# Performance work log

Hardware: AMD Instinct MI355X
Metric: run time of the kernel (lower is better)

## Reference

```python
import jax, jax.numpy as jnp
import numpy as np
from jax import lax

NUM_SIMS = 2048
NUM_BITS = 256   # == num_nodes
MID_DIM = 512
LN_EPS = 1e-5


def _net(x, w1, b1, gamma, beta, w2, b2):
    # BnMLP: Linear -> GELU (exact erf) -> LayerNorm -> Linear -> Sigmoid
    h = x @ w1 + b1                                   # [S, MID]
    h = jax.nn.gelu(h, approximate=False)
    mu = jnp.mean(h, axis=-1, keepdims=True)
    var = jnp.mean(jnp.square(h - mu), axis=-1, keepdims=True)
    h = (h - mu) * lax.rsqrt(var + LN_EPS) * gamma + beta
    return jax.nn.sigmoid(h @ w2 + b2)                # [S, NUM_BITS]


def setup_inputs() -> dict:
    key = jax.random.key(0)
    k_x, k_p, k_w1, k_w2 = jax.random.split(key, 4)
    xs_flt = jax.random.uniform(k_x, (NUM_SIMS, NUM_BITS), dtype=jnp.float32)
    # one random permutation of the nodes per simulation (th.randperm per sim)
    ids_ary = jax.vmap(lambda k: jax.random.permutation(k, NUM_BITS))(
        jax.random.split(k_p, NUM_SIMS)).astype(jnp.int32)   # [S, N]
    w1 = jax.random.normal(k_w1, (NUM_BITS, MID_DIM), jnp.float32) / np.sqrt(NUM_BITS)
    b1 = jnp.full((MID_DIM,), 1e-6, jnp.float32)
    gamma = jnp.ones((MID_DIM,), jnp.float32)
    beta = jnp.zeros((MID_DIM,), jnp.float32)
    w2 = jax.random.normal(k_w2, (MID_DIM, NUM_BITS), jnp.float32) * (0.1 / np.sqrt(MID_DIM))
    b2 = jnp.full((NUM_BITS,), 1e-6, jnp.float32)
    return {"xs_flt": xs_flt, "ids_ary": ids_ary, "w1": w1, "b1": b1,
            "gamma": gamma, "beta": beta, "w2": w2, "b2": b2}


def reference(xs_flt, ids_ary, w1, b1, gamma, beta, w2, b2):
    # gathers prob at (sim, ids[sim]) and writes ps broadcast over all rows at
    # columns ids (faithful to torch's `probs[:, ids] = ps` broadcast semantics).
    def step(probs, ids):
        out = _net(probs, w1, b1, gamma, beta, w2, b2)        # [S, N]
        ps = jnp.take_along_axis(out, ids[:, None], axis=1)[:, 0]  # [S]
        probs = probs.at[:, ids].set(ps)                      # broadcast over rows
        return probs, None

    probs, _ = lax.scan(step, xs_flt, ids_ary.T)              # scan over N nodes
    return probs
```

## Files before the change

kernel.cpp:

```cpp
#include <hip/hip_runtime.h>
#include <math.h>

#define S_ 2048
#define N_ 256
#define MID_ 512
#define NB_ 8
#define JSL_ 64
#define LN_EPS_ 1e-5f
#define NBLK_ 64
#define NSTEP_ 253
#define BSTRIDE_ 288
#define SLOT_F_ (NB_*BSTRIDE_)
#define TAGST_ 16
#define TAG_TARGET_ 0x0101010101010101ULL

typedef float f32x4 __attribute__((ext_vector_type(4)));
typedef float f32x2 __attribute__((ext_vector_type(2)));

__device__ __forceinline__ float gelu_exact(float x){
    return 0.5f * x * (1.0f + erff(x * 0.70710678118654752440f));
}


__global__ __launch_bounds__(256) void k_setup(
    const int* __restrict__ ids, const float* __restrict__ gamma,
    const float* __restrict__ beta, const float* __restrict__ w2,
    const float* __restrict__ b2,
    unsigned int* __restrict__ wmaskb, int* __restrict__ winners,
    float* __restrict__ A, float* __restrict__ Bc,
    int* __restrict__ tagw32, int* __restrict__ cnt, int* __restrict__ winner)
{
    __shared__ float ra[256], rb[256];
    __shared__ unsigned int mb[8];
    __shared__ int lk[N_];
    int bi = blockIdx.x, tid = threadIdx.x;

    if (tid < 32){
        int ii = bi*32 + tid;
        if (ii < NSTEP_*TAGST_*2) tagw32[ii] = 0;
    }
    if (bi == 0 && tid < 8) cnt[tid] = 0;
    if (bi == 0 && tid == 0) *winner = -1;

    if (tid < 8) mb[tid] = 0u;
    lk[tid] = -1;
    __syncthreads();
    #pragma unroll
    for (int m = 0; m < 8; m++){
        int k = tid + m*256;
        int c = ids[k*N_ + bi];
        atomicOr(&mb[c>>5], 1u << (c&31));
        if (bi < 3) atomicMax(&lk[c], k);
    }
    float a = 0.f, b = 0.f;
    for (int j = tid; j < MID_; j += 256){
        float v = w2[j*N_ + bi];
        a += gamma[j]*v;
        b += beta[j]*v;
    }
    ra[tid] = a; rb[tid] = b;
    __syncthreads();
    for (int off = 128; off > 0; off >>= 1){
        if (tid < off){ ra[tid] += ra[tid+off]; rb[tid] += rb[tid+off]; }
        __syncthreads();
    }
    if (tid == 0){ A[bi] = ra[0]; Bc[bi] = rb[0] + b2[bi]; }
    if (tid < 8) wmaskb[bi*8 + tid] = mb[tid];
    if (bi < 3) winners[bi*N_ + tid] = lk[tid];
}


__global__ __launch_bounds__(256) void k_fullW(
    const float* __restrict__ xs, const float* __restrict__ w1,
    const float* __restrict__ b1, const float* __restrict__ gamma,
    const float* __restrict__ beta, const float* __restrict__ w2,
    const float* __restrict__ b2, const int* __restrict__ winners,
    float* __restrict__ nv, int t)
{
    __shared__ float prow[4][N_];
    int tid = threadIdx.x;
    int r = tid >> 6, l = tid & 63;
    int c = blockIdx.x*4 + r;
    int kr = winners[t*N_ + c];
    int krow = kr < 0 ? 0 : kr;
    #pragma unroll
    for (int q = 0; q < 4; q++){
        int cc = l*4 + q;
        float v = xs[krow*N_ + cc];
        if (t > 0 && winners[cc] >= 0)      v = nv[cc];
        if (t > 1 && winners[N_ + cc] >= 0) v = nv[N_ + cc];
        prow[r][cc] = v;
    }
    float h[8];
    #pragma unroll
    for (int m = 0; m < 8; m++) h[m] = b1[l + 64*m];
    for (int cc = 0; cc < N_; cc++){
        float p = prow[r][cc];
        const float* w1r = w1 + cc*MID_;
        #pragma unroll
        for (int m = 0; m < 8; m++) h[m] = fmaf(p, w1r[l + 64*m], h[m]);
    }
    float s1 = 0.f, s2 = 0.f;
    #pragma unroll
    for (int m = 0; m < 8; m++){
        float g = gelu_exact(h[m]);
        h[m] = g; s1 += g; s2 += g*g;
    }
    #pragma unroll
    for (int off = 32; off > 0; off >>= 1){
        s1 += __shfl_xor(s1, off, 64);
        s2 += __shfl_xor(s2, off, 64);
    }
    float mu  = s1 * (1.f/MID_);
    float var = s2 * (1.f/MID_) - mu*mu;
    float inv = rsqrtf(var + LN_EPS_);
    float acc = 0.f;
    #pragma unroll
    for (int m = 0; m < 8; m++){
        int j = l + 64*m;
        float hn = (h[m] - mu)*inv*gamma[j] + beta[j];
        acc = fmaf(hn, w2[j*N_ + c], acc);
    }
    #pragma unroll
    for (int off = 32; off > 0; off >>= 1) acc += __shfl_xor(acc, off, 64);
    if (l == 0) nv[t*N_ + c] = 1.f/(1.f + expf(-(acc + b2[c])));
}


__global__ __launch_bounds__(512) void k_fast(
    const float* __restrict__ w1, const float* __restrict__ b1,
    const float* __restrict__ gamma, const float* __restrict__ w2,
    const float* __restrict__ A, const float* __restrict__ Bc,
    const unsigned int* __restrict__ wmaskb, const float* __restrict__ xs,
    const int* __restrict__ winners3, const float* __restrict__ nv,
    float* __restrict__ slots, unsigned long long* __restrict__ tagw,
    int* __restrict__ cnt, int* __restrict__ winner,
    float* __restrict__ out, int t0)
{
    __shared__ int s_role;
    __shared__ __attribute__((aligned(16))) float commonS[N_];
    __shared__ __attribute__((aligned(16))) float gvals[JSL_];
    __shared__ __attribute__((aligned(16))) float crow[N_];
    __shared__ float ws8[16];
    __shared__ float pst[NB_][2];
    __shared__ unsigned int wbits[(N_*N_)/32];

    int tid = threadIdx.x;

    if (tid == 0){
        int xcd;
        asm volatile("s_getreg_b32 %0, hwreg(HW_REG_XCC_ID)" : "=s"(xcd));
        xcd &= 7;
        int pos = atomicAdd(&cnt[xcd], 1);
        int role = -1;
        if (pos == NB_ - 1){
            int old = atomicCAS(winner, -1, xcd);
            if (old == -1) role = NB_ - 1;
        } else if (pos < NB_ - 1){
            int w;
            while ((w = atomicCAS(winner, -2, -2)) == -1)
                __builtin_amdgcn_s_sleep(2);
            if (w == xcd) role = pos;
        }
        s_role = role;
    }
    __syncthreads();
    int role = s_role;
    if (role < 0) return;
    int j0 = role * JSL_;

    int l = tid & 63, w = tid >> 6;
    int cg = l & 7;
    int jA = (w<<3) + (l>>3);
    int cB = w*32 + (l & 31);
    int khalf = l >> 5;

    float w1r[32];
    #pragma unroll
    for (int cc = 0; cc < 32; cc++)
        w1r[cc] = w1[(cg*32 + cc)*MID_ + j0 + jA];
    float g2r[32];
    #pragma unroll
    for (int kk = 0; kk < 32; kk++)
        g2r[kk] = gamma[j0 + khalf*32 + kk] * w2[(j0 + khalf*32 + kk)*N_ + cB];
    float b1v = b1[j0 + jA];

    for (int i = tid; i < (N_*N_)/32; i += 512) wbits[i] = wmaskb[i];
    if (tid < N_){
        float v = xs[tid];
        if (winners3[tid] >= 0)        v = nv[tid];
        if (winners3[N_ + tid] >= 0)   v = nv[N_ + tid];
        if (winners3[2*N_ + tid] >= 0) v = nv[2*N_ + tid];
        commonS[tid ^ (((tid>>5)&7)<<2)] = v;
    }
    float Ac  = (tid < N_) ? A[tid]  : 0.f;
    float Bcc = (tid < N_) ? Bc[tid] : 0.f;
    __syncthreads();

    for (int t = t0; t < N_; t++){
        int si = t - t0;
        float* slot = slots + si*SLOT_F_;
        float* myp  = slot + role*BSTRIDE_;
        {
            float a0=0.f, a1=0.f, a2=0.f, a3=0.f;
            #pragma unroll
            for (int cc = 0; cc < 8; cc++){
                f32x4 cv = *(const f32x4*)(&commonS[(cg*32 + cc*4) ^ (cg<<2)]);
                a0 = fmaf(w1r[cc*4+0], cv.x, a0);
                a1 = fmaf(w1r[cc*4+1], cv.y, a1);
                a2 = fmaf(w1r[cc*4+2], cv.z, a2);
                a3 = fmaf(w1r[cc*4+3], cv.w, a3);
            }
            float hp = (a0+a1) + (a2+a3);
            hp += __shfl_xor(hp, 1);
            hp += __shfl_xor(hp, 2);
            hp += __shfl_xor(hp, 4);
            float g = gelu_exact(hp + b1v);
            float s1 = g, s2 = g*g;
            s1 += __shfl_xor(s1, 8);  s2 += __shfl_xor(s2, 8);
            s1 += __shfl_xor(s1, 16); s2 += __shfl_xor(s2, 16);
            s1 += __shfl_xor(s1, 32); s2 += __shfl_xor(s2, 32);
            if (l == 0){ ws8[w*2] = s1; ws8[w*2+1] = s2; }
            if (cg == 0) gvals[jA] = g;
        }
        __syncthreads();
        {
            float p0=0.f, p1=0.f, p2=0.f, p3=0.f;
            #pragma unroll
            for (int kk = 0; kk < 8; kk++){
                f32x4 gv = *(const f32x4*)(&gvals[khalf*32 + kk*4]);
                p0 = fmaf(g2r[kk*4+0], gv.x, p0);
                p1 = fmaf(g2r[kk*4+1], gv.y, p1);
                p2 = fmaf(g2r[kk*4+2], gv.z, p2);
                p3 = fmaf(g2r[kk*4+3], gv.w, p3);
            }
            float p = (p0+p1) + (p2+p3);
            p += __shfl_xor(p, 32);
            if (l < 32) myp[cB] = p;
        }
        if (tid == 0){
            float S1 = 0.f, S2 = 0.f;
            #pragma unroll
            for (int ww = 0; ww < 8; ww++){ S1 += ws8[ww*2]; S2 += ws8[ww*2+1]; }
            f32x2 st; st.x = S1; st.y = S2;
            *(f32x2*)(myp + 256) = st;
        }
        asm volatile("s_waitcnt vmcnt(0)" ::: "memory");
        __syncthreads();
        {
            unsigned long long* tp = tagw + si*TAGST_;
            if (tid == 0) atomicAdd(tp, 1ULL << (8*role));
            if (tid < NB_){
                while (atomicAdd(tp, 0ULL) != TAG_TARGET_) {}
                f32x2 st = *(const f32x2*)(slot + tid*BSTRIDE_ + 256);
                pst[tid][0] = st.x; pst[tid][1] = st.y;
            }
        }
        __syncthreads();
        if (tid < N_){
            const float* sp = slot + tid;
            float s1 = 0.f;
            #pragma unroll
            for (int bb = 0; bb < NB_; bb++) s1 += sp[bb*BSTRIDE_];
            float S1 = 0.f, S2 = 0.f;
            #pragma unroll
            for (int bb = 0; bb < NB_; bb++){ S1 += pst[bb][0]; S2 += pst[bb][1]; }
            float mu  = S1 * (1.f/MID_);
            float var = S2 * (1.f/MID_) - mu*mu;
            float inv = rsqrtf(var + LN_EPS_);
            float s = inv*(s1 - mu*Ac) + Bcc;
            float o = 1.f/(1.f + expf(-s));
            if ((wbits[(t<<3) + (tid>>5)] >> (tid&31)) & 1u)
                commonS[tid ^ (((tid>>5)&7)<<2)] = o;
        }
        __syncthreads();
    }
    if (tid < N_) crow[tid] = commonS[tid ^ (((tid>>5)&7)<<2)];
    __syncthreads();
    {
        float* obase = out + (role*256)*N_;
        for (int i = tid; i < 256*(N_/4); i += 512){
            int rr = i >> 6, v4 = i & 63;
            *(f32x4*)(&obase[rr*N_ + v4*4]) = *(const f32x4*)(&crow[v4*4]);
        }
    }
}


extern "C" void kernel_launch(void* const* d_in, const int* in_sizes, int n_in,
                              void* d_out, int out_size, void* d_ws, size_t ws_size,
                              hipStream_t stream)
{
    const float* xs    = (const float*)d_in[0];
    const int*   ids   = (const int*)  d_in[1];
    const float* w1    = (const float*)d_in[2];
    const float* b1    = (const float*)d_in[3];
    const float* gamma = (const float*)d_in[4];
    const float* beta  = (const float*)d_in[5];
    const float* w2    = (const float*)d_in[6];
    const float* b2    = (const float*)d_in[7];
    float* out = (float*)d_out;

    float* ws      = (float*)d_ws;
    float* slots   = ws;
    float* nv      = ws + 582912;
    float* A       = ws + 583680;
    float* Bc      = ws + 583936;
    int*   winners = (int*)(ws + 584192);
    unsigned int* wmaskb = (unsigned int*)(ws + 584960);
    int*   tagw32  = (int*)(ws + 587008);
    unsigned long long* tagw = (unsigned long long*)tagw32;
    int*   cnt     = tagw32 + NSTEP_*TAGST_*2;
    int*   winner  = cnt + 8;

    k_setup<<<256, 256, 0, stream>>>(ids, gamma, beta, w2, b2, wmaskb, winners,
                                     A, Bc, tagw32, cnt, winner);

    for (int t = 0; t < 3; t++)
        k_fullW<<<64, 256, 0, stream>>>(xs, w1, b1, gamma, beta, w2, b2,
                                        winners, nv, t);

    k_fast<<<NBLK_, 512, 0, stream>>>(w1, b1, gamma, w2, A, Bc, wmaskb, xs,
                                      winners, nv, slots, tagw, cnt, winner,
                                      out, 3);
}
```

Measured before the change: 637.6 us.

## Reduce per-step partials with float atomics into one shared row

Each of the 8 cooperating blocks used to write its partial second-layer sums and LayerNorm statistics to a private slot. Readers then waited on a byte-packed tag and summed all 8 slots. Now every block atomically adds into a single accumulator row per step, signals an int counter, and each consuming wave spins on the counter itself, which removes one block-wide barrier. This cuts the per-step gather latency and barrier count on the sequential critical path, at the cost of contended float atomics and a non-deterministic summation order.

```diff
diff --git a/kernel.cpp b/kernel.cpp
--- a/kernel.cpp
+++ b/kernel.cpp
@@ -9,10 +9,8 @@
 #define LN_EPS_ 1e-5f
 #define NBLK_ 64
 #define NSTEP_ 253
-#define BSTRIDE_ 288
-#define SLOT_F_ (NB_*BSTRIDE_)
-#define TAGST_ 16
-#define TAG_TARGET_ 0x0101010101010101ULL
+#define AROW_ 288
+#define TAGW_ 32
 
 typedef float f32x4 __attribute__((ext_vector_type(4)));
 typedef float f32x2 __attribute__((ext_vector_type(2)));
@@ -28,17 +26,16 @@
     const float* __restrict__ b2,
     unsigned int* __restrict__ wmaskb, int* __restrict__ winners,
     float* __restrict__ A, float* __restrict__ Bc,
-    int* __restrict__ tagw32, int* __restrict__ cnt, int* __restrict__ winner)
+    float* __restrict__ accum, int* __restrict__ tagw32,
+    int* __restrict__ cnt, int* __restrict__ winner)
 {
     __shared__ float ra[256], rb[256];
     __shared__ unsigned int mb[8];
     __shared__ int lk[N_];
     int bi = blockIdx.x, tid = threadIdx.x;
 
-    if (tid < 32){
-        int ii = bi*32 + tid;
-        if (ii < NSTEP_*TAGST_*2) tagw32[ii] = 0;
-    }
+    for (int ii = bi*256 + tid; ii < NSTEP_*AROW_; ii += 256*256) accum[ii] = 0.f;
+    for (int ii = bi*256 + tid; ii < NSTEP_*TAGW_; ii += 256*256) tagw32[ii] = 0;
     if (bi == 0 && tid < 8) cnt[tid] = 0;
     if (bi == 0 && tid == 0) *winner = -1;
 
@@ -133,7 +130,7 @@
     const float* __restrict__ A, const float* __restrict__ Bc,
     const unsigned int* __restrict__ wmaskb, const float* __restrict__ xs,
     const int* __restrict__ winners3, const float* __restrict__ nv,
-    float* __restrict__ slots, unsigned long long* __restrict__ tagw,
+    float* __restrict__ accum, int* __restrict__ tagw32,
     int* __restrict__ cnt, int* __restrict__ winner,
     float* __restrict__ out, int t0)
 {
@@ -142,7 +139,6 @@
     __shared__ __attribute__((aligned(16))) float gvals[JSL_];
     __shared__ __attribute__((aligned(16))) float crow[N_];
     __shared__ float ws8[16];
-    __shared__ float pst[NB_][2];
     __shared__ unsigned int wbits[(N_*N_)/32];
 
     int tid = threadIdx.x;
@@ -199,8 +195,7 @@
 
     for (int t = t0; t < N_; t++){
         int si = t - t0;
-        float* slot = slots + si*SLOT_F_;
-        float* myp  = slot + role*BSTRIDE_;
+        float* arow = accum + si*AROW_;
         {
             float a0=0.f, a1=0.f, a2=0.f, a3=0.f;
             #pragma unroll
@@ -236,37 +231,29 @@
             }
             float p = (p0+p1) + (p2+p3);
             p += __shfl_xor(p, 32);
-            if (l < 32) myp[cB] = p;
+            if (l < 32) atomicAdd(&arow[cB], p);
         }
         if (tid == 0){
             float S1 = 0.f, S2 = 0.f;
             #pragma unroll
             for (int ww = 0; ww < 8; ww++){ S1 += ws8[ww*2]; S2 += ws8[ww*2+1]; }
-            f32x2 st; st.x = S1; st.y = S2;
-            *(f32x2*)(myp + 256) = st;
+            atomicAdd(&arow[256], S1);
+            atomicAdd(&arow[257], S2);
         }
         asm volatile("s_waitcnt vmcnt(0)" ::: "memory");
         __syncthreads();
         {
-            unsigned long long* tp = tagw + si*TAGST_;
-            if (tid == 0) atomicAdd(tp, 1ULL << (8*role));
-            if (tid < NB_){
-                while (atomicAdd(tp, 0ULL) != TAG_TARGET_) {}
-                f32x2 st = *(const f32x2*)(slot + tid*BSTRIDE_ + 256);
-                pst[tid][0] = st.x; pst[tid][1] = st.y;
+            int* tp = tagw32 + si*TAGW_;
+            if (tid == 0) atomicAdd(tp, 1);
+            if (w < 4 && l == 0){
+                while (atomicAdd(tp, 0) < NB_) {}
             }
         }
-        __syncthreads();
         if (tid < N_){
-            const float* sp = slot + tid;
-            float s1 = 0.f;
-            #pragma unroll
-            for (int bb = 0; bb < NB_; bb++) s1 += sp[bb*BSTRIDE_];
-            float S1 = 0.f, S2 = 0.f;
-            #pragma unroll
-            for (int bb = 0; bb < NB_; bb++){ S1 += pst[bb][0]; S2 += pst[bb][1]; }
-            float mu  = S1 * (1.f/MID_);
-            float var = S2 * (1.f/MID_) - mu*mu;
+            float s1 = arow[tid];
+            f32x2 st = *(const f32x2*)(arow + 256);
+            float mu  = st.x * (1.f/MID_);
+            float var = st.y * (1.f/MID_) - mu*mu;
             float inv = rsqrtf(var + LN_EPS_);
             float s = inv*(s1 - mu*Ac) + Bcc;
             float o = 1.f/(1.f + expf(-s));
@@ -302,25 +289,24 @@
     float* out = (float*)d_out;
 
     float* ws      = (float*)d_ws;
-    float* slots   = ws;
-    float* nv      = ws + 582912;
-    float* A       = ws + 583680;
-    float* Bc      = ws + 583936;
-    int*   winners = (int*)(ws + 584192);
-    unsigned int* wmaskb = (unsigned int*)(ws + 584960);
-    int*   tagw32  = (int*)(ws + 587008);
-    unsigned long long* tagw = (unsigned long long*)tagw32;
-    int*   cnt     = tagw32 + NSTEP_*TAGST_*2;
+    float* accum   = ws;
+    float* nv      = ws + 72864;
+    float* A       = ws + 73632;
+    float* Bc      = ws + 73888;
+    int*   winners = (int*)(ws + 74144);
+    unsigned int* wmaskb = (unsigned int*)(ws + 74912);
+    int*   tagw32  = (int*)(ws + 76960);
+    int*   cnt     = tagw32 + NSTEP_*TAGW_;
     int*   winner  = cnt + 8;
 
     k_setup<<<256, 256, 0, stream>>>(ids, gamma, beta, w2, b2, wmaskb, winners,
-                                     A, Bc, tagw32, cnt, winner);
+                                     A, Bc, accum, tagw32, cnt, winner);
 
     for (int t = 0; t < 3; t++)
         k_fullW<<<64, 256, 0, stream>>>(xs, w1, b1, gamma, beta, w2, b2,
                                         winners, nv, t);
 
     k_fast<<<NBLK_, 512, 0, stream>>>(w1, b1, gamma, w2, A, Bc, wmaskb, xs,
-                                      winners, nv, slots, tagw, cnt, winner,
+                                      winners, nv, accum, tagw32, cnt, winner,
                                       out, 3);
 }
```

Result: slower. 681.3 us (+6.9%).
